# Performance work log

Measured on AMD Instinct MI355X. Metric: run time of the kernel, lower is better.

The kernel has to match this reference:

```python
import jax, jax.numpy as jnp
import numpy as np

G_DIMS = [30, 30, 24, 18, 18]
G_DOWN = [10, 10, 8, 6, 6]
S_DIM = 10
N_OBJ = 45
N_STREAMS = 5
P_DIM = sum(G_DOWN) * S_DIM          # 400
HID = 20 * S_DIM                     # 200
FREQS = np.array([0.01, 0.7, 0.91, 0.97, 0.99], dtype=np.float32)
DECAY, N_ITERS = 0.8, 5
HEB_LR, HEB_FORGET = 0.5, 0.9999
LOGSIG_RATIO, LOGSIG_OFFSET = 6.0, -2.0
B, T = 256, 8
_G_OFFS = np.concatenate([[0], np.cumsum(G_DIMS)]).astype(int)


def _leaky_clamp(x):
    # f(clamp(x, -1, 1)) with f = leaky_relu (torch default slope 0.01)
    return jax.nn.leaky_relu(jnp.clip(x, -1.0, 1.0))


def _scale_log_sigma(raw, temp=1.0):
    return LOGSIG_OFFSET + temp * jnp.tanh(raw / LOGSIG_RATIO) * LOGSIG_RATIO


def _downsample(g):  # [B, 120] -> [B, 40]; take first g_down dims of each stream
    return jnp.concatenate([g[:, o:o + d] for o, d in zip(_G_OFFS[:-1], G_DOWN)], axis=1)


def setup_inputs() -> dict:
    key = jax.random.key(0)
    ks = jax.random.split(key, 10)
    return {
        "g_seq": jax.random.normal(ks[0], (B, T, sum(G_DIMS)), jnp.float32),
        "x_idx": jax.random.randint(ks[1], (B, T), 0, N_OBJ),
        "W_comp": jax.random.normal(ks[2], (N_OBJ, S_DIM), jnp.float32) * 0.3,
        "W_repeat": jax.random.normal(ks[3], (P_DIM, sum(G_DOWN)), jnp.float32) * 0.2,
        "W_tile": jax.random.normal(ks[4], (P_DIM, N_STREAMS * S_DIM), jnp.float32) * 0.2,
        "W_tile0": jax.random.normal(ks[5], (G_DOWN[0] * S_DIM, S_DIM), jnp.float32) * 0.2,
        "w_x": jnp.ones((), jnp.float32),
        "b_x": jnp.zeros((S_DIM,), jnp.float32),
        "W1": jax.random.normal(ks[6], (S_DIM, HID), jnp.float32) * 0.2,
        "b1": jnp.zeros((HID,), jnp.float32),
        "W2": jax.random.normal(ks[7], (HID, N_OBJ), jnp.float32) * 0.1,
        "b2": jnp.zeros((N_OBJ,), jnp.float32),
        "W_lv1": jax.random.normal(ks[8], (P_DIM, P_DIM), jnp.float32) * 0.05,
        "b_lv1": jnp.zeros((P_DIM,), jnp.float32),
        "W_lv2": jax.random.normal(ks[9], (P_DIM, P_DIM), jnp.float32) * 0.05,
        "b_lv2": jnp.zeros((P_DIM,), jnp.float32),
    }


def _forward(g_seq, x_onehot, W_comp, W_repeat, W_tile, W_tile0, w_x, b_x,
             W1, b1, W2, b2, W_lv1, b_lv1, W_lv2, b_lv2):
    Bn = g_seq.shape[0]
    freqs = jnp.asarray(FREQS, dtype=g_seq.dtype)

    def step(carry, xs):
        M, x_filt = carry            # M: [B,P,P] Hebbian memory; x_filt: [B,5,10]
        g_t, x_t = xs                # g_t: [B,120], x_t: [B,45]
        # sensory compression + per-stream exponential temporal filtering
        x_c = x_t @ W_comp                                          # [B,10]
        x_filt = (1.0 - freqs)[None, :, None] * x_filt + freqs[None, :, None] * x_c[:, None, :]
        x_flat = x_filt.reshape(Bn, N_STREAMS * S_DIM)              # [B,50]
        # fused p-vector formation (_scriptable_fused_form_p)
        g_down = _downsample(g_t)                                   # [B,40]
        g_exp = g_down @ W_repeat.T                                 # [B,400]
        x_exp = x_flat @ W_tile.T                                   # [B,400]
        p_inf = _leaky_clamp(g_exp * x_exp)
        # attractor retrieval seeded from g projected to p-space (_scriptable_transform_g_to_p)
        h = _leaky_clamp(g_exp)
        for _ in range(N_ITERS):                                    # memory_iterations
            h = _leaky_clamp(DECAY * h + jnp.einsum('bij,bj->bi', M, h))
        p_ret = h
        # precision-weighted Gaussian fusion of inference and memory estimates
        lv1 = _scale_log_sigma(p_inf @ W_lv1 + b_lv1)
        lv2 = _scale_log_sigma(p_ret @ W_lv2 + b_lv2)
        inv1, inv2 = jnp.exp(-lv1), jnp.exp(-lv2)
        var_c = 1.0 / (inv1 + inv2)
        p_t = var_c * (p_inf * inv1 + p_ret * inv2)
        # Hebbian update: M <- lambda*M + eta*(p - p_hat)(p + p_hat)^T
        M = HEB_FORGET * M + HEB_LR * jnp.einsum('bi,bj->bij', p_t - p_ret, p_t + p_ret)
        # generative decode from stream-0 slice of p (GenerativeNetwork.forward_decode)
        x_s = w_x * (p_t[:, :G_DOWN[0] * S_DIM] @ W_tile0) + b_x    # [B,10]
        logits = jax.nn.elu(x_s @ W1 + b1) @ W2 + b2                # [B,45]
        return (M, x_filt), logits

    M0 = jnp.zeros((Bn, P_DIM, P_DIM), g_seq.dtype)
    xf0 = jnp.zeros((Bn, N_STREAMS, S_DIM), g_seq.dtype)
    xs = (jnp.swapaxes(g_seq, 0, 1), jnp.swapaxes(x_onehot, 0, 1))
    _, logits = jax.lax.scan(step, (M0, xf0), xs)                   # [T,B,45]
    return jnp.swapaxes(logits, 0, 1)                               # [B,T,45]


def reference(g_seq, x_idx, W_comp, W_repeat, W_tile, W_tile0, w_x, b_x,
              W1, b1, W2, b2, W_lv1, b_lv1, W_lv2, b_lv2):
    x_onehot = jax.nn.one_hot(x_idx, N_OBJ, dtype=g_seq.dtype)
    return _forward(g_seq, x_onehot, W_comp, W_repeat, W_tile, W_tile0, w_x, b_x,
                    W1, b1, W2, b2, W_lv1, b_lv1, W_lv2, b_lv2)
```

## Files before the change

kernel.cpp:

```cpp
#include <hip/hip_runtime.h>

#define kT 8
#define kG 120
#define kP 400
#define kObj 45
#define kS 10
#define kHid 200

__device__ __constant__ int c_gmap[40] = {
    0,1,2,3,4,5,6,7,8,9,
    30,31,32,33,34,35,36,37,38,39,
    60,61,62,63,64,65,66,67,
    84,85,86,87,88,89,
    102,103,104,105,106,107};

__device__ __constant__ float c_freq[5] = {0.01f, 0.7f, 0.91f, 0.97f, 0.99f};

__device__ __forceinline__ float leaky_clamp(float x) {
    x = fminf(fmaxf(x, -1.0f), 1.0f);
    return x > 0.0f ? x : 0.01f * x;
}

__global__ __launch_bounds__(512) void tem_kernel(
    const float* __restrict__ g_seq, const int* __restrict__ x_idx,
    const float* __restrict__ W_comp, const float* __restrict__ W_repeat,
    const float* __restrict__ W_tile, const float* __restrict__ W_tile0,
    const float* __restrict__ w_x, const float* __restrict__ b_x,
    const float* __restrict__ W1, const float* __restrict__ b1,
    const float* __restrict__ W2, const float* __restrict__ b2,
    const float* __restrict__ W_lv1, const float* __restrict__ b_lv1,
    const float* __restrict__ W_lv2, const float* __restrict__ b_lv2,
    float* __restrict__ out)
{
    const int b   = blockIdx.x;
    const int tid = threadIdx.x;
    const int dim = tid;
    const bool hasD = (tid < kP);
    const int wid  = tid >> 6;
    const int lane = tid & 63;
    const int g   = tid >> 7;
    const int r   = tid & 127;
    const bool mact = (r < 100);
    const int j0  = g * 100;

    __shared__ __align__(16) float pT[kP][kT];
    __shared__ __align__(16) float hT[kP][kT];
    __shared__ __align__(16) float lvT[kP][kT];
    __shared__ __align__(16) float xfT[50][kT];
    __shared__ __align__(16) float gdT[40][kT];
    __shared__ float s_h[kP];
    __shared__ float s_pt[kP];
    __shared__ float s_u[kT][kP];
    __shared__ float s_v[kT][kP];
    __shared__ __align__(16) float s_part[4][kP];
    __shared__ float s_red[2][kT][8];
    __shared__ int   s_idx[kT];
    __shared__ float s_xsp[kS][kS];
    __shared__ float s_xs[kS];
    __shared__ float s_hid[kHid];
    __shared__ float s_lp[8][kObj];

    const float blv1 = hasD ? b_lv1[dim] : 0.0f;
    const float blv2 = hasD ? b_lv2[dim] : 0.0f;
    const float wx   = w_x[0];

    if (tid < kT) s_idx[tid] = x_idx[b * kT + tid];
    __syncthreads();

    if (tid < 40) {
        int gi = c_gmap[tid];
        #pragma unroll
        for (int t = 0; t < kT; ++t)
            gdT[tid][t] = g_seq[(b * kT + t) * kG + gi];
    } else if (tid >= 64 && tid < 114) {
        int rr = tid - 64, d = rr % 10;
        float f = c_freq[rr / 10];
        float xf = 0.0f;
        #pragma unroll
        for (int t = 0; t < kT; ++t) {
            float xc = W_comp[s_idx[t] * kS + d];
            xf = (1.0f - f) * xf + f * xc;
            xfT[rr][t] = xf;
        }
    }
    __syncthreads();

    if (hasD) {
        float ge[kT], xe[kT];
        #pragma unroll
        for (int t = 0; t < kT; ++t) { ge[t] = 0.0f; xe[t] = 0.0f; }
        for (int j = 0; j < 40; ++j) {
            float w = W_repeat[dim * 40 + j];
            float4 gA = *(const float4*)&gdT[j][0];
            float4 gB = *(const float4*)&gdT[j][4];
            ge[0] += w * gA.x; ge[1] += w * gA.y; ge[2] += w * gA.z; ge[3] += w * gA.w;
            ge[4] += w * gB.x; ge[5] += w * gB.y; ge[6] += w * gB.z; ge[7] += w * gB.w;
        }
        for (int j = 0; j < 50; ++j) {
            float w = W_tile[dim * 50 + j];
            float4 xA = *(const float4*)&xfT[j][0];
            float4 xB = *(const float4*)&xfT[j][4];
            xe[0] += w * xA.x; xe[1] += w * xA.y; xe[2] += w * xA.z; xe[3] += w * xA.w;
            xe[4] += w * xB.x; xe[5] += w * xB.y; xe[6] += w * xB.z; xe[7] += w * xB.w;
        }
        float4 pA, pB, hA, hB;
        pA.x = leaky_clamp(ge[0] * xe[0]); pA.y = leaky_clamp(ge[1] * xe[1]);
        pA.z = leaky_clamp(ge[2] * xe[2]); pA.w = leaky_clamp(ge[3] * xe[3]);
        pB.x = leaky_clamp(ge[4] * xe[4]); pB.y = leaky_clamp(ge[5] * xe[5]);
        pB.z = leaky_clamp(ge[6] * xe[6]); pB.w = leaky_clamp(ge[7] * xe[7]);
        hA.x = leaky_clamp(ge[0]); hA.y = leaky_clamp(ge[1]);
        hA.z = leaky_clamp(ge[2]); hA.w = leaky_clamp(ge[3]);
        hB.x = leaky_clamp(ge[4]); hB.y = leaky_clamp(ge[5]);
        hB.z = leaky_clamp(ge[6]); hB.w = leaky_clamp(ge[7]);
        *(float4*)&pT[dim][0] = pA; *(float4*)&pT[dim][4] = pB;
        *(float4*)&hT[dim][0] = hA; *(float4*)&hT[dim][4] = hB;
    }
    __syncthreads();

    if (hasD) {
        float acc[kT];
        #pragma unroll
        for (int t = 0; t < kT; ++t) acc[t] = 0.0f;
        #pragma unroll 4
        for (int j = 0; j < kP; ++j) {
            float w = W_lv1[j * kP + dim];
            float4 pA = *(const float4*)&pT[j][0];
            float4 pB = *(const float4*)&pT[j][4];
            acc[0] += w * pA.x; acc[1] += w * pA.y; acc[2] += w * pA.z; acc[3] += w * pA.w;
            acc[4] += w * pB.x; acc[5] += w * pB.y; acc[6] += w * pB.z; acc[7] += w * pB.w;
        }
        *(float4*)&lvT[dim][0] = make_float4(acc[0], acc[1], acc[2], acc[3]);
        *(float4*)&lvT[dim][4] = make_float4(acc[4], acc[5], acc[6], acc[7]);
    }
    __syncthreads();

    int par = 0;
    for (int t = 0; t < kT; ++t) {
        float h = hasD ? hT[dim][t] : 0.0f;
        if (t == 0) {
            #pragma unroll
            for (int it = 0; it < 5; ++it) h = leaky_clamp(0.8f * h);
        } else {
            for (int it = 0; it < 5; ++it) {
                for (int s = 0; s < t; ++s) {
                    float p = hasD ? s_v[s][dim] * h : 0.0f;
                    #pragma unroll
                    for (int off = 32; off; off >>= 1) p += __shfl_down(p, off, 64);
                    if (lane == 0) s_red[par][s][wid] = p;
                }
                __syncthreads();
                if (hasD) {
                    float mh = 0.0f;
                    float c = 0.5f;
                    for (int s = t - 1; s >= 0; --s) {
                        float d = 0.0f;
                        #pragma unroll
                        for (int w = 0; w < 8; ++w) d += s_red[par][s][w];
                        mh += c * d * s_u[s][dim];
                        c *= 0.9999f;
                    }
                    h = leaky_clamp(0.8f * h + mh);
                }
                par ^= 1;
            }
        }
        if (hasD) s_h[dim] = h;
        __syncthreads();

        if (mact) {
            float4 a0{0,0,0,0}, a1{0,0,0,0}, a2{0,0,0,0}, a3{0,0,0,0};
            #pragma unroll 2
            for (int jj = 0; jj < 100; jj += 4) {
                int j = j0 + jj;
                float4 w0 = ((const float4*)(W_lv2 + (j+0) * kP))[r];
                float4 w1v = ((const float4*)(W_lv2 + (j+1) * kP))[r];
                float4 w2v = ((const float4*)(W_lv2 + (j+2) * kP))[r];
                float4 w3 = ((const float4*)(W_lv2 + (j+3) * kP))[r];
                float v0 = s_h[j+0], v1 = s_h[j+1], v2 = s_h[j+2], v3 = s_h[j+3];
                a0.x += w0.x * v0; a0.y += w0.y * v0; a0.z += w0.z * v0; a0.w += w0.w * v0;
                a1.x += w1v.x * v1; a1.y += w1v.y * v1; a1.z += w1v.z * v1; a1.w += w1v.w * v1;
                a2.x += w2v.x * v2; a2.y += w2v.y * v2; a2.z += w2v.z * v2; a2.w += w2v.w * v2;
                a3.x += w3.x * v3; a3.y += w3.y * v3; a3.z += w3.z * v3; a3.w += w3.w * v3;
            }
            float4 tot;
            tot.x = (a0.x + a1.x) + (a2.x + a3.x);
            tot.y = (a0.y + a1.y) + (a2.y + a3.y);
            tot.z = (a0.z + a1.z) + (a2.z + a3.z);
            tot.w = (a0.w + a1.w) + (a2.w + a3.w);
            ((float4*)&s_part[g][0])[r] = tot;
        }
        __syncthreads();

        if (hasD) {
            float lv2raw = (s_part[0][dim] + s_part[1][dim])
                         + (s_part[2][dim] + s_part[3][dim]) + blv2;
            float lv1raw = lvT[dim][t] + blv1;
            float l1 = -2.0f + 6.0f * tanhf(lv1raw * (1.0f / 6.0f));
            float l2 = -2.0f + 6.0f * tanhf(lv2raw * (1.0f / 6.0f));
            float i1v = expf(-l1), i2v = expf(-l2);
            float pinf = pT[dim][t];
            float p = (pinf * i1v + h * i2v) / (i1v + i2v);
            s_pt[dim] = p;
            s_u[t][dim] = p - h;
            s_v[t][dim] = p + h;
        }
        __syncthreads();

        if (tid < 100) {
            int d = tid % 10, c = tid / 10;
            float acc = 0.0f;
            #pragma unroll
            for (int jj = 0; jj < 10; ++jj) {
                int j = c * 10 + jj;
                acc += s_pt[j] * W_tile0[j * kS + d];
            }
            s_xsp[c][d] = acc;
        }
        __syncthreads();
        if (tid < kS) {
            float acc = 0.0f;
            #pragma unroll
            for (int c = 0; c < 10; ++c) acc += s_xsp[c][tid];
            s_xs[tid] = wx * acc + b_x[tid];
        }
        __syncthreads();
        if (tid < kHid) {
            float acc = b1[tid];
            #pragma unroll
            for (int d = 0; d < kS; ++d)
                acc += s_xs[d] * W1[d * kHid + tid];
            s_hid[tid] = acc > 0.0f ? acc : (expf(acc) - 1.0f);
        }
        __syncthreads();
        if (tid < 360) {
            int o = tid % kObj, c = tid / kObj;
            float acc = 0.0f;
            #pragma unroll
            for (int hh = 0; hh < 25; ++hh) {
                int hI = c * 25 + hh;
                acc += s_hid[hI] * W2[hI * kObj + o];
            }
            s_lp[c][o] = acc;
        }
        __syncthreads();
        if (tid < kObj) {
            float acc = b2[tid];
            #pragma unroll
            for (int c = 0; c < 8; ++c) acc += s_lp[c][tid];
            out[(b * kT + t) * kObj + tid] = acc;
        }
        __syncthreads();
    }
}

extern "C" void kernel_launch(void* const* d_in, const int* in_sizes, int n_in,
                              void* d_out, int out_size, void* d_ws, size_t ws_size,
                              hipStream_t stream) {
    const float* g_seq   = (const float*)d_in[0];
    const int*   x_idx   = (const int*)d_in[1];
    const float* W_comp  = (const float*)d_in[2];
    const float* W_repeat= (const float*)d_in[3];
    const float* W_tile  = (const float*)d_in[4];
    const float* W_tile0 = (const float*)d_in[5];
    const float* w_x     = (const float*)d_in[6];
    const float* b_x     = (const float*)d_in[7];
    const float* W1      = (const float*)d_in[8];
    const float* b1      = (const float*)d_in[9];
    const float* W2      = (const float*)d_in[10];
    const float* b2      = (const float*)d_in[11];
    const float* W_lv1   = (const float*)d_in[12];
    const float* b_lv1   = (const float*)d_in[13];
    const float* W_lv2   = (const float*)d_in[14];
    const float* b_lv2   = (const float*)d_in[15];
    float* out = (float*)d_out;

    const int Bn = in_sizes[0] / (kT * kG);
    tem_kernel<<<dim3(Bn), dim3(512), 0, stream>>>(
        g_seq, x_idx, W_comp, W_repeat, W_tile, W_tile0, w_x, b_x,
        W1, b1, W2, b2, W_lv1, b_lv1, W_lv2, b_lv2, out);
}
```

Before: 249.3 us.

## Cache part of W_lv2 in registers and shared memory across timesteps

Preloads the first 32 rows of each thread's W_lv2 slice into registers and the next 12 rows into shared memory once before the time loop. The per-step matvec then reads those rows from on-chip storage and streams only the remaining rows from global memory. This cuts repeated global/L2 traffic for W_lv2 over the 8 steps, but adds 128 registers per thread and about 77KB of LDS. Together with launch bounds that request 2 blocks per CU, that risks register spills or reduced occupancy.

Result: slower. 354.3 us (+42.1%).

```diff
diff --git a/kernel.cpp b/kernel.cpp
--- a/kernel.cpp
+++ b/kernel.cpp
@@ -6,6 +6,9 @@
 #define kObj 45
 #define kS 10
 #define kHid 200
+#define NV 32
+#define NL 12
+#define NC (NV + NL)
 
 __device__ __constant__ int c_gmap[40] = {
     0,1,2,3,4,5,6,7,8,9,
@@ -21,7 +24,7 @@
     return x > 0.0f ? x : 0.01f * x;
 }
 
-__global__ __launch_bounds__(512) void tem_kernel(
+__global__ __launch_bounds__(512, 2) void tem_kernel(
     const float* __restrict__ g_seq, const int* __restrict__ x_idx,
     const float* __restrict__ W_comp, const float* __restrict__ W_repeat,
     const float* __restrict__ W_tile, const float* __restrict__ W_tile0,
@@ -48,6 +51,7 @@
     __shared__ __align__(16) float lvT[kP][kT];
     __shared__ __align__(16) float xfT[50][kT];
     __shared__ __align__(16) float gdT[40][kT];
+    __shared__ __align__(16) float s_wc[4][NL][kP];
     __shared__ float s_h[kP];
     __shared__ float s_pt[kP];
     __shared__ float s_u[kT][kP];
@@ -66,6 +70,17 @@
 
     if (tid < kT) s_idx[tid] = x_idx[b * kT + tid];
     __syncthreads();
+
+    float4 wreg[NV];
+    if (mact) {
+        #pragma unroll
+        for (int k = 0; k < NV; ++k)
+            wreg[k] = ((const float4*)(W_lv2 + (j0 + k) * kP))[r];
+        #pragma unroll
+        for (int k = 0; k < NL; ++k)
+            ((float4*)&s_wc[g][k][0])[r] =
+                ((const float4*)(W_lv2 + (j0 + NV + k) * kP))[r];
+    }
 
     if (tid < 40) {
         int gi = c_gmap[tid];
@@ -169,8 +184,29 @@
 
         if (mact) {
             float4 a0{0,0,0,0}, a1{0,0,0,0}, a2{0,0,0,0}, a3{0,0,0,0};
+            #pragma unroll
+            for (int k = 0; k < NV; k += 4) {
+                float v0 = s_h[j0+k], v1 = s_h[j0+k+1], v2 = s_h[j0+k+2], v3 = s_h[j0+k+3];
+                a0.x += wreg[k].x * v0; a0.y += wreg[k].y * v0; a0.z += wreg[k].z * v0; a0.w += wreg[k].w * v0;
+                a1.x += wreg[k+1].x * v1; a1.y += wreg[k+1].y * v1; a1.z += wreg[k+1].z * v1; a1.w += wreg[k+1].w * v1;
+                a2.x += wreg[k+2].x * v2; a2.y += wreg[k+2].y * v2; a2.z += wreg[k+2].z * v2; a2.w += wreg[k+2].w * v2;
+                a3.x += wreg[k+3].x * v3; a3.y += wreg[k+3].y * v3; a3.z += wreg[k+3].z * v3; a3.w += wreg[k+3].w * v3;
+            }
+            #pragma unroll
+            for (int k = 0; k < NL; k += 4) {
+                int j = j0 + NV + k;
+                float4 w0 = ((const float4*)&s_wc[g][k+0][0])[r];
+                float4 w1v = ((const float4*)&s_wc[g][k+1][0])[r];
+                float4 w2v = ((const float4*)&s_wc[g][k+2][0])[r];
+                float4 w3 = ((const float4*)&s_wc[g][k+3][0])[r];
+                float v0 = s_h[j+0], v1 = s_h[j+1], v2 = s_h[j+2], v3 = s_h[j+3];
+                a0.x += w0.x * v0; a0.y += w0.y * v0; a0.z += w0.z * v0; a0.w += w0.w * v0;
+                a1.x += w1v.x * v1; a1.y += w1v.y * v1; a1.z += w1v.z * v1; a1.w += w1v.w * v1;
+                a2.x += w2v.x * v2; a2.y += w2v.y * v2; a2.z += w2v.z * v2; a2.w += w2v.w * v2;
+                a3.x += w3.x * v3; a3.y += w3.y * v3; a3.z += w3.z * v3; a3.w += w3.w * v3;
+            }
             #pragma unroll 2
-            for (int jj = 0; jj < 100; jj += 4) {
+            for (int jj = NC; jj < 100; jj += 4) {
                 int j = j0 + jj;
                 float4 w0 = ((const float4*)(W_lv2 + (j+0) * kP))[r];
                 float4 w1v = ((const float4*)(W_lv2 + (j+1) * kP))[r];
```
